# Kernel optimization log

Hardware: AMD Instinct MI355X
Metric: run time of the kernel (lower is better)

## Reference

```python
import jax, jax.numpy as jnp
import numpy as np

B, T, S, A, H = 64, 128, 100, 16, 120
TAU = 5.0


def setup_inputs() -> dict:
    key = jax.random.key(0)
    ks = jax.random.split(key, 12)
    kH = 1.0 / np.sqrt(H)
    u = lambda k, shape, b: jax.random.uniform(k, shape, jnp.float32, -b, b)
    return {
        "x": jax.random.normal(ks[0], (B, T, S, A), jnp.float32),
        # PyTorch LSTM params (gate order i, f, g, o), uniform(-1/sqrt(H), 1/sqrt(H))
        "W_ih": u(ks[1], (4 * H, A), kH),
        "W_hh": u(ks[2], (4 * H, H), kH),
        "b_ih": u(ks[3], (4 * H,), kH),
        "b_hh": u(ks[4], (4 * H,), kH),
        # score head: Linear(H, 1)
        "w_lin": u(ks[5], (1, H), kH),
        "b_lin": u(ks[6], (1,), kH),
        # MLP: Linear(S*S, 256), Linear(256, S)
        "W2": u(ks[7], (256, S * S), 1.0 / np.sqrt(S * S)),
        "b2": u(ks[8], (256,), 1.0 / np.sqrt(S * S)),
        "W3": u(ks[9], (S, 256), 1.0 / np.sqrt(256)),
        "b3": u(ks[10], (S,), 1.0 / np.sqrt(256)),
    }


def reference(x, W_ih, W_hh, b_ih, b_hh, w_lin, b_lin, W2, b2, W3, b3):
    Bsz, Tlen, Ns, _ = x.shape
    Hd = W_hh.shape[1]
    # Batch all stocks together: original loops the LSTM per stock with zero init,
    # which is mathematically identical to one LSTM over batch B*S.
    xr = jnp.transpose(x, (1, 0, 2, 3)).reshape(Tlen, Bsz * Ns, -1)  # (T, B*S, A)
    bias = b_ih + b_hh

    def step(carry, xt):
        h, c = carry
        g = xt @ W_ih.T + h @ W_hh.T + bias          # (B*S, 4H)
        i, f, gg, o = jnp.split(g, 4, axis=-1)
        i = jax.nn.sigmoid(i)
        f = jax.nn.sigmoid(f)
        gg = jnp.tanh(gg)
        o = jax.nn.sigmoid(o)
        c = f * c + i * gg
        h = o * jnp.tanh(c)
        return (h, c), None

    h0 = jnp.zeros((Bsz * Ns, Hd), x.dtype)
    (h_last, _), _ = jax.lax.scan(step, (h0, h0), xr)
    lstm_out_last = h_last.reshape(Bsz, Ns, Hd)       # (B, S, H)

    # per-element score linear (batched instead of python double-loop)
    s = lstm_out_last @ w_lin.T + b_lin               # (B, S, 1)

    # NeuralSort relaxed permutation matrix, tau = 5
    A_s = jnp.abs(s - jnp.transpose(s, (0, 2, 1)))    # (B, S, S)
    rowsum = A_s.sum(axis=-1, keepdims=True)          # (B, S, 1) == A_s @ 1 1^T rows
    scaling = (Ns + 1 - 2 * jnp.arange(1, Ns + 1)).astype(x.dtype)  # (S,)
    C = s * scaling[None, None, :]                    # (B, S, S)
    P_max = jnp.transpose(C - rowsum, (0, 2, 1))
    p_hat = jax.nn.softmax(P_max / TAU, axis=-1)      # (B, S, S)

    foo = p_hat.reshape(Bsz, Ns * Ns)
    z = jax.nn.relu(foo @ W2.T + b2)
    z = z @ W3.T + b3
    return jax.nn.softmax(z, axis=-1)                 # (B, S)
```

## Files before the change

### kernel.cpp

```cpp
#include <hip/hip_runtime.h>
#include <hip/hip_bf16.h>
#include <cstddef>

#define NSTOCK 100
#define LOG2E 1.4426950408889634f

typedef _Float16 f16x8 __attribute__((ext_vector_type(8)));
typedef _Float16 f16x4 __attribute__((ext_vector_type(4)));
typedef float f32x16 __attribute__((ext_vector_type(16)));

static __device__ __forceinline__ float rcpf(float x){ return __builtin_amdgcn_rcpf(x); }
static __device__ __forceinline__ float exp2f_(float x){ return __builtin_amdgcn_exp2f(x); }

__global__ void prep_kernel(const float* __restrict__ W_ih,
                            const float* __restrict__ W_hh,
                            const float* __restrict__ b_ih,
                            const float* __restrict__ b_hh,
                            float* __restrict__ Wp) {
    int idx = blockIdx.x * 256 + threadIdx.x;
    if (idx < 480 * 144) {
        int k = idx % 144;
        int p = idx / 144;
        int n = p >> 5, row = p & 31, jjf = row >> 2, type = row & 3;
        int j = n * 8 + (jjf & 1) * 4 + (jjf >> 1);
        int g = type * 120 + j;
        float scale = (type == 2) ? 2.f * LOG2E : -LOG2E;
        float v = 0.f;
        if (k < 136)       v = ((k < 16) ? W_ih[g * 16 + k] : W_hh[g * 120 + (k - 16)]) * scale;
        else if (k == 136) v = (b_ih[g] + b_hh[g]) * scale;
        Wp[idx] = v;
    }
}

__global__ __launch_bounds__(1024) void lstm_kernel(
        const float* __restrict__ x,
        const float* __restrict__ Wp,
        const float* __restrict__ w_lin,
        const float* __restrict__ b_lin,
        float* __restrict__ s_out) {
    __shared__ __align__(16) _Float16 AHi[2][9][64][8];
    __shared__ float sred[30][32];

    const int tid   = threadIdx.x;
    const int lane  = tid & 63;
    const int w     = tid >> 6;
    const int l31   = lane & 31;
    const int lhalf = lane >> 5;
    const int n0    = blockIdx.x * 32;

    f16x8 bh[9];
    if (w < 15) {
        const int p = w * 32 + l31;
#pragma unroll
        for (int kt = 0; kt < 9; ++kt) {
            const float* wp = Wp + p * 144 + kt * 16 + lhalf * 8;
            f16x8 hi;
#pragma unroll
            for (int e = 0; e < 8; ++e) hi[e] = (_Float16)wp[e];
            bh[kt] = hi;
        }
    }

    {
        f16x8 z;
#pragma unroll
        for (int e = 0; e < 8; ++e) z[e] = (_Float16)0.f;
        int bf = tid >> 9, kt = 1 + ((tid >> 6) & 7), ln = tid & 63;
        *(f16x8*)&AHi[bf][kt][ln][0] = z;
    }
    __syncthreads();

    const int bx = lane >> 1;
    const int hx = lane & 1;
    const int nx  = n0 + bx;
    const int bbx = nx / NSTOCK, ssx = nx % NSTOCK;
    const float* xbase = x + (size_t)bbx * 204800 + ssx * 16 + hx * 8;
    if (w == 15) {
        float4 a0 = *(const float4*)xbase;
        float4 a1 = *(const float4*)(xbase + 4);
        float vv[8] = {a0.x, a0.y, a0.z, a0.w, a1.x, a1.y, a1.z, a1.w};
        f16x8 hi;
#pragma unroll
        for (int e = 0; e < 8; ++e) hi[e] = (_Float16)vv[e];
        *(f16x8*)&AHi[0][0][bx + 32 * hx][0] = hi;
    }
    if (tid < 64) {
        int buf = tid >> 5, b = tid & 31;
        AHi[buf][8][32 + b][0] = (_Float16)1.f;
    }
    __syncthreads();

    const int ktw = 1 + (w >> 1);
    const int lnw = l31 + 32 * (w & 1);
    const int e0  = 4 * lhalf;

    float creg[4] = {0.f, 0.f, 0.f, 0.f};
    float hlast[4] = {0.f, 0.f, 0.f, 0.f};

    for (int t = 0; t < 128; ++t) {
        const int rb = t & 1;
        const int wb = rb ^ 1;
        if (w == 15) {
            int tt = (t < 127) ? t + 1 : 127;
            const float* xp = xbase + (size_t)tt * 1600;
            float4 a0 = *(const float4*)xp;
            float4 a1 = *(const float4*)(xp + 4);
            float vv[8] = {a0.x, a0.y, a0.z, a0.w, a1.x, a1.y, a1.z, a1.w};
            f16x8 hi;
#pragma unroll
            for (int e = 0; e < 8; ++e) hi[e] = (_Float16)vv[e];
            *(f16x8*)&AHi[wb][0][bx + 32 * hx][0] = hi;
        } else {
            f16x8 afr[9];
#pragma unroll
            for (int kt = 0; kt < 9; ++kt)
                afr[kt] = *(const f16x8*)&AHi[rb][kt][lane][0];
            f32x16 acc;
#pragma unroll
            for (int r = 0; r < 16; ++r) acc[r] = 0.f;
#pragma unroll
            for (int kt = 0; kt < 9; ++kt)
                acc = __builtin_amdgcn_mfma_f32_32x32x16_f16(bh[kt], afr[kt], acc, 0, 0, 0);
            f16x4 hi4;
#pragma unroll
            for (int p = 0; p < 4; ++p) {
                float iv = rcpf(1.f + exp2f_(acc[4 * p + 0]));
                float fv = rcpf(1.f + exp2f_(acc[4 * p + 1]));
                float gv = 1.f - 2.f * rcpf(1.f + exp2f_(acc[4 * p + 2]));
                float ov = rcpf(1.f + exp2f_(acc[4 * p + 3]));
                float c = fv * creg[p] + iv * gv;
                creg[p] = c;
                float h = ov * (1.f - 2.f * rcpf(1.f + exp2f_(c * 2.8853900817779268f)));
                hlast[p] = h;
                hi4[p] = (_Float16)h;
            }
            *(f16x4*)&AHi[wb][ktw][lnw][e0] = hi4;
        }
        __syncthreads();
    }

    if (w < 15) {
        const int jb = w * 8 + 4 * lhalf;
        float sp = 0.f;
#pragma unroll
        for (int p = 0; p < 4; ++p) sp += w_lin[jb + p] * hlast[p];
        sred[w * 2 + lhalf][l31] = sp;
    }
    __syncthreads();
    if (tid < 32) {
        float s = b_lin[0];
#pragma unroll
        for (int r = 0; r < 30; ++r) s += sred[r][tid];
        s_out[n0 + tid] = s;
    }
}

__global__ __launch_bounds__(128) void phat_kernel(const float* __restrict__ s,
                                                   float* __restrict__ fooT) {
    __shared__ float a[NSTOCK], c[NSTOCK];
    const int b = blockIdx.x >> 1, half = blockIdx.x & 1, tid = threadIdx.x;
    const float* sb = s + b * NSTOCK;
    if (tid < NSTOCK) {
        float sj = sb[tid];
        float rs = 0.f;
        for (int i2 = 0; i2 < NSTOCK; ++i2) rs += fabsf(sj - sb[i2]);
        a[tid] = sj * 0.2f;
        c[tid] = rs * 0.2f;
    }
    __syncthreads();
    if (tid < 50) {
        const int i = half * 50 + tid;
        const float sci = (float)(99 - 2 * i);
        float m = -1e30f;
        for (int j = 0; j < NSTOCK; ++j) m = fmaxf(m, sci * a[j] - c[j]);
        float sum = 0.f;
        for (int j = 0; j < NSTOCK; ++j) sum += __expf(sci * a[j] - c[j] - m);
        const float inv = 1.f / sum;
        for (int j = 0; j < NSTOCK; ++j)
            fooT[(size_t)(i * NSTOCK + j) * 64 + b] = __expf(sci * a[j] - c[j] - m) * inv;
    }
}

__global__ __launch_bounds__(512) void mlp1_kernel(const float* __restrict__ fooT,
                                                   const float* __restrict__ W2,
                                                   float* __restrict__ z2Tp) {
    __shared__ float part[8][4][64];
    const int tid = threadIdx.x;
    const int wv = tid >> 6, lane = tid & 63;
    const int ug = blockIdx.x >> 1, half = blockIdx.x & 1;
    const int u0 = ug * 4;
    const int m0 = half * 5000 + wv * 625;
    float a0 = 0.f, a1 = 0.f, a2 = 0.f, a3 = 0.f;
    for (int mi = 0; mi < 625; ++mi) {
        int m = m0 + mi;
        float v = fooT[(size_t)m * 64 + lane];
        a0 += v * W2[(size_t)(u0 + 0) * 10000 + m];
        a1 += v * W2[(size_t)(u0 + 1) * 10000 + m];
        a2 += v * W2[(size_t)(u0 + 2) * 10000 + m];
        a3 += v * W2[(size_t)(u0 + 3) * 10000 + m];
    }
    part[wv][0][lane] = a0; part[wv][1][lane] = a1;
    part[wv][2][lane] = a2; part[wv][3][lane] = a3;
    __syncthreads();
    if (tid < 256) {
        int q = tid >> 6, b = tid & 63;
        float s = 0.f;
#pragma unroll
        for (int w2 = 0; w2 < 8; ++w2) s += part[w2][q][b];
        z2Tp[((size_t)half * 256 + (u0 + q)) * 64 + b] = s;
    }
}

__global__ __launch_bounds__(128) void mlp2_kernel(const float* __restrict__ z2Tp,
                                                   const float* __restrict__ b2,
                                                   const float* __restrict__ W3,
                                                   const float* __restrict__ b3,
                                                   float* __restrict__ out) {
    __shared__ float zs[256];
    __shared__ float logits[NSTOCK];
    const int b = blockIdx.x, tid = threadIdx.x;
    for (int u = tid; u < 256; u += 128) {
        float v = b2[u] + z2Tp[(size_t)u * 64 + b] + z2Tp[(size_t)(256 + u) * 64 + b];
        zs[u] = fmaxf(v, 0.f);
    }
    __syncthreads();
    if (tid < NSTOCK) {
        float acc = b3[tid];
        const float* wr = W3 + tid * 256;
        for (int u = 0; u < 256; ++u) acc += zs[u] * wr[u];
        logits[tid] = acc;
    }
    __syncthreads();
    if (tid < NSTOCK) {
        float m = -1e30f;
        for (int j = 0; j < NSTOCK; ++j) m = fmaxf(m, logits[j]);
        float sum = 0.f;
        for (int j = 0; j < NSTOCK; ++j) sum += __expf(logits[j] - m);
        out[b * NSTOCK + tid] = __expf(logits[tid] - m) / sum;
    }
}

extern "C" void kernel_launch(void* const* d_in, const int* in_sizes, int n_in,
                              void* d_out, int out_size, void* d_ws, size_t ws_size,
                              hipStream_t stream) {
    const float* x     = (const float*)d_in[0];
    const float* W_ih  = (const float*)d_in[1];
    const float* W_hh  = (const float*)d_in[2];
    const float* b_ih  = (const float*)d_in[3];
    const float* b_hh  = (const float*)d_in[4];
    const float* w_lin = (const float*)d_in[5];
    const float* b_lin = (const float*)d_in[6];
    const float* W2    = (const float*)d_in[7];
    const float* b2    = (const float*)d_in[8];
    const float* W3    = (const float*)d_in[9];
    const float* b3    = (const float*)d_in[10];

    float* ws    = (float*)d_ws;
    float* Wp    = ws;
    float* sbuf  = ws + 69600;
    float* fooT  = ws + 76000;
    float* z2Tp  = ws + 716000;
    float* out   = (float*)d_out;

    prep_kernel<<<271, 256, 0, stream>>>(W_ih, W_hh, b_ih, b_hh, Wp);
    lstm_kernel<<<200, 1024, 0, stream>>>(x, Wp, w_lin, b_lin, sbuf);
    phat_kernel<<<128, 128, 0, stream>>>(sbuf, fooT);
    mlp1_kernel<<<128, 512, 0, stream>>>(fooT, W2, z2Tp);
    mlp2_kernel<<<64, 128, 0, stream>>>(z2Tp, b2, W3, b3, out);
}
```

Before: 244.7 us.

## Store p_hat in fp16 and give mlp1 blocks eight units over a quarter of K

The softmax matrix p_hat is now written as half precision, which halves the intermediate buffer traffic between phat and mlp1. mlp1 is repartitioned so each block handles 8 output units over a quarter of the 10000-long reduction instead of 4 units over half. This doubles reuse of each loaded p_hat value per W2 read. mlp2 now sums four partial results instead of two. fp16 storage of probabilities adds some rounding error.

```diff
diff --git a/kernel.cpp b/kernel.cpp
--- a/kernel.cpp
+++ b/kernel.cpp
@@ -156,7 +156,7 @@
 }
 
 __global__ __launch_bounds__(128) void phat_kernel(const float* __restrict__ s,
-                                                   float* __restrict__ fooT) {
+                                                   _Float16* __restrict__ fooT16) {
     __shared__ float a[NSTOCK], c[NSTOCK];
     const int b = blockIdx.x >> 1, half = blockIdx.x & 1, tid = threadIdx.x;
     const float* sb = s + b * NSTOCK;
@@ -177,37 +177,40 @@
         for (int j = 0; j < NSTOCK; ++j) sum += __expf(sci * a[j] - c[j] - m);
         const float inv = 1.f / sum;
         for (int j = 0; j < NSTOCK; ++j)
-            fooT[(size_t)(i * NSTOCK + j) * 64 + b] = __expf(sci * a[j] - c[j] - m) * inv;
-    }
-}
-
-__global__ __launch_bounds__(512) void mlp1_kernel(const float* __restrict__ fooT,
+            fooT16[(size_t)(i * NSTOCK + j) * 64 + b] =
+                (_Float16)(__expf(sci * a[j] - c[j] - m) * inv);
+    }
+}
+
+__global__ __launch_bounds__(512) void mlp1_kernel(const _Float16* __restrict__ fooT16,
                                                    const float* __restrict__ W2,
                                                    float* __restrict__ z2Tp) {
-    __shared__ float part[8][4][64];
+    __shared__ float part[8][8][64];
     const int tid = threadIdx.x;
     const int wv = tid >> 6, lane = tid & 63;
-    const int ug = blockIdx.x >> 1, half = blockIdx.x & 1;
-    const int u0 = ug * 4;
-    const int m0 = half * 5000 + wv * 625;
-    float a0 = 0.f, a1 = 0.f, a2 = 0.f, a3 = 0.f;
-    for (int mi = 0; mi < 625; ++mi) {
-        int m = m0 + mi;
-        float v = fooT[(size_t)m * 64 + lane];
-        a0 += v * W2[(size_t)(u0 + 0) * 10000 + m];
-        a1 += v * W2[(size_t)(u0 + 1) * 10000 + m];
-        a2 += v * W2[(size_t)(u0 + 2) * 10000 + m];
-        a3 += v * W2[(size_t)(u0 + 3) * 10000 + m];
-    }
-    part[wv][0][lane] = a0; part[wv][1][lane] = a1;
-    part[wv][2][lane] = a2; part[wv][3][lane] = a3;
-    __syncthreads();
-    if (tid < 256) {
-        int q = tid >> 6, b = tid & 63;
+    const int ug = blockIdx.x >> 2, q = blockIdx.x & 3;
+    const int u0 = ug * 8;
+    const int cnt   = (wv < 4) ? 313 : 312;
+    const int start = q * 2500 + wv * 312 + ((wv < 4) ? wv : 4);
+    float a[8];
+#pragma unroll
+    for (int qq = 0; qq < 8; ++qq) a[qq] = 0.f;
+    for (int mi = 0; mi < cnt; ++mi) {
+        int m = start + mi;
+        float v = (float)fooT16[(size_t)m * 64 + lane];
+#pragma unroll
+        for (int qq = 0; qq < 8; ++qq)
+            a[qq] += v * W2[(size_t)(u0 + qq) * 10000 + m];
+    }
+#pragma unroll
+    for (int qq = 0; qq < 8; ++qq) part[wv][qq][lane] = a[qq];
+    __syncthreads();
+    {
+        int qq = tid >> 6, b = tid & 63;
         float s = 0.f;
 #pragma unroll
-        for (int w2 = 0; w2 < 8; ++w2) s += part[w2][q][b];
-        z2Tp[((size_t)half * 256 + (u0 + q)) * 64 + b] = s;
+        for (int w2 = 0; w2 < 8; ++w2) s += part[w2][qq][b];
+        z2Tp[((size_t)q * 256 + (u0 + qq)) * 64 + b] = s;
     }
 }
 
@@ -220,7 +223,11 @@
     __shared__ float logits[NSTOCK];
     const int b = blockIdx.x, tid = threadIdx.x;
     for (int u = tid; u < 256; u += 128) {
-        float v = b2[u] + z2Tp[(size_t)u * 64 + b] + z2Tp[(size_t)(256 + u) * 64 + b];
+        float v = b2[u]
+                + z2Tp[(size_t)u * 64 + b]
+                + z2Tp[(size_t)(256 + u) * 64 + b]
+                + z2Tp[(size_t)(512 + u) * 64 + b]
+                + z2Tp[(size_t)(768 + u) * 64 + b];
         zs[u] = fmaxf(v, 0.f);
     }
     __syncthreads();
@@ -258,13 +265,13 @@
     float* ws    = (float*)d_ws;
     float* Wp    = ws;
     float* sbuf  = ws + 69600;
-    float* fooT  = ws + 76000;
-    float* z2Tp  = ws + 716000;
+    _Float16* fooT16 = (_Float16*)(ws + 76000);
+    float* z2Tp  = ws + 396000;
     float* out   = (float*)d_out;
 
     prep_kernel<<<271, 256, 0, stream>>>(W_ih, W_hh, b_ih, b_hh, Wp);
     lstm_kernel<<<200, 1024, 0, stream>>>(x, Wp, w_lin, b_lin, sbuf);
-    phat_kernel<<<128, 128, 0, stream>>>(sbuf, fooT);
-    mlp1_kernel<<<128, 512, 0, stream>>>(fooT, W2, z2Tp);
+    phat_kernel<<<128, 128, 0, stream>>>(sbuf, fooT16);
+    mlp1_kernel<<<128, 512, 0, stream>>>(fooT16, W2, z2Tp);
     mlp2_kernel<<<64, 128, 0, stream>>>(z2Tp, b2, W3, b3, out);
 }
```

Measured after the change: 289.8 us. 1.18x slower.
